# Performance work log

Hardware: AMD Instinct MI355X
Metric: run time of the kernel (lower is better)

## Reference

```python
import jax, jax.numpy as jnp
import numpy as np

B, S, D, HW = 256, 32, 512, 196


def setup_inputs() -> dict:
    key = jax.random.key(0)
    ks = jax.random.split(key, 34)
    n = lambda k, sh, s=1.0: jax.random.normal(k, sh, dtype=jnp.float32) * s
    w = 0.03  # xavier-ish scale for D=512 layers
    return {
        "words": n(ks[0], (B, S, D)),
        "question": n(ks[1], (B, 2 * D)),
        "know": n(ks[2], (B, D, HW)),
        "control0": n(ks[3], (B, D)),
        "memory0": n(ks[4], (B, D)),
        # ControlUnit
        "Wsc": n(ks[5], (2 * D, D), w), "bsc": jnp.zeros((D,), jnp.float32),
        "Wp": n(ks[6], (D, D), w), "bp": jnp.zeros((D,), jnp.float32),
        "Wcq": n(ks[7], (2 * D, D), w), "bcq": jnp.zeros((D,), jnp.float32),
        "wac": n(ks[8], (D, 1), w), "bac": jnp.zeros((1,), jnp.float32),
        # ReadUnit
        "Wm": n(ks[9], (D, D), w), "bm": jnp.zeros((D,), jnp.float32),
        "Wk": n(ks[10], (D, D), w), "bk": jnp.zeros((D,), jnp.float32),
        "Wc1": n(ks[11], (3 * D, D), w), "bc1": jnp.zeros((D,), jnp.float32),
        "Wc2": n(ks[12], (D, D), w), "bc2": jnp.zeros((D,), jnp.float32),
        "war": n(ks[13], (D, 1), w), "bar": jnp.zeros((1,), jnp.float32),
        # WriteUnit (self-attention variant)
        "Wwc": n(ks[14], (D, D), w), "bwc": jnp.zeros((D,), jnp.float32),
        "waw": n(ks[15], (D, 1), w), "baw": jnp.zeros((1,), jnp.float32),
        "Wwcat": n(ks[16], (3 * D, D), w), "bwcat": jnp.zeros((D,), jnp.float32),
    }


def reference(words, question, know, control0, memory0,
              Wsc, bsc, Wp, bp, Wcq, bcq, wac, bac,
              Wm, bm, Wk, bk, Wc1, bc1, Wc2, bc2, war, bar,
              Wwc, bwc, waw, baw, Wwcat, bwcat):
    # ---- ControlUnit (step 0) ----
    q = jnp.tanh(question @ Wsc + bsc)                    # [B,D]
    pa = q @ Wp + bp                                      # position_aware[0]
    cq = jnp.concatenate([control0, pa], axis=1) @ Wcq + bcq  # [B,D]
    logit_c = (cq[:, None, :] * words) @ wac + bac        # [B,S,1]
    attn_c = jax.nn.softmax(logit_c, axis=1)
    control = jnp.sum(attn_c * words, axis=1)             # [B,D]

    # ---- ReadUnit ----
    pm = memory0 @ Wm + bm                                # [B,D]
    pk = jnp.einsum('bdn,de->ben', know, Wk) + bk[None, :, None]  # [B,D,HW]
    pm_b = jnp.broadcast_to(pm[:, :, None], pk.shape)
    feat = jnp.concatenate([pm_b * pk, pk, pm_b], axis=1)  # [B,3D,HW]
    h = jax.nn.relu(jnp.einsum('bfn,fd->bnd', feat, Wc1) + bc1)  # [B,HW,D]
    h = h @ Wc2 + bc2                                     # [B,HW,D]
    logit_r = (h * control[:, None, :]) @ war + bar       # [B,HW,1]
    a_r = jax.nn.softmax(logit_r[..., 0], axis=1)          # [B,HW]
    read = jnp.einsum('bdn,bn->bd', know, a_r)            # [B,D]

    # ---- WriteUnit (self-attention over previous controls; T=1 at step 0) ----
    sc = control @ Wwc + bwc                              # [B,D]
    ctrl_prev = control0[:, :, None]                      # [B,D,T]
    logit_w = jnp.einsum('bdt,d->bt', sc[:, :, None] * ctrl_prev, waw[:, 0]) + baw  # [B,T]
    a_w = jax.nn.softmax(logit_w, axis=1)
    attn_mem = jnp.einsum('bdt,bt->bd', memory0[:, :, None], a_w)  # [B,D]
    concat = jnp.concatenate([read, memory0, attn_mem], axis=1)    # [B,3D]
    next_mem = concat @ Wwcat + bwcat                     # [B,D]

    return control, next_mem
```

## Files before the change

kernel.cpp:

```cpp
#include <hip/hip_runtime.h>
#include <hip/hip_bf16.h>
#include <math.h>

typedef __hip_bfloat16 bf16;
typedef __attribute__((ext_vector_type(8))) short s8v;
typedef __attribute__((ext_vector_type(4))) float f4v;

#define BB 256
#define SS 32
#define DD 512
#define HWN 196
#define AP 40

__device__ __forceinline__ float b2f(bf16 x){ return __bfloat162float(x); }
__device__ __forceinline__ bf16 f2b(float x){ return __float2bfloat16(x); }
__device__ __forceinline__ float us2f(unsigned short u){
    union { unsigned int i; float f; } t; t.i = ((unsigned int)u) << 16; return t.f;
}
template<int DT>
__device__ __forceinline__ float ldin(const void* p, size_t i){
    return DT ? b2f(((const bf16*)p)[i]) : ((const float*)p)[i];
}

__global__ void detect_k(const void* q, int* flag){
    __shared__ int cnt;
    if (threadIdx.x == 0) cnt = 0;
    __syncthreads();
    const unsigned short* u = (const unsigned short*)q;
    unsigned short v = u[threadIdx.x * 4];
    int e = (v >> 7) & 0xFF;
    atomicAdd(&cnt, (e >= 100 && e <= 140) ? 1 : 0);
    __syncthreads();
    if (threadIdx.x == 0) *flag = (cnt > 128) ? 1 : 0;
}

struct PJob { const void* s; const void* s2; bf16* d; int R, C, ldd, kofs, mode, nblk, boff; };
struct PrepP { PJob j[11]; const void* war; const void* bk; float* warf; float* bkf; };

template<int DT>
__global__ __launch_bounds__(256) void prep_k(PrepP P, const int* __restrict__ flag){
    if (*flag != DT) return;
    __shared__ float T[32][33];
    int bx = blockIdx.x;
    int ji = 0;
    #pragma unroll
    for (int i = 0; i < 11; ++i) if (bx >= P.j[i].boff) ji = i;
    PJob jb = P.j[ji];
    int t = bx - jb.boff;
    int tx = threadIdx.x & 31, ty = threadIdx.x >> 5;
    if (jb.mode == 3){
        for (int i = threadIdx.x; i < DD; i += 256){
            P.warf[i] = ldin<DT>(P.war, i);
            P.bkf[i]  = ldin<DT>(P.bk, i);
        }
        return;
    }
    int nrt = jb.R >> 5;
    int r0 = (t % nrt) << 5, c0 = (t / nrt) << 5;
    if (jb.mode == 2){
        for (int rr = ty; rr < 32; rr += 8)
            jb.d[(size_t)(r0 + rr) * jb.ldd + jb.kofs + c0 + tx] =
                f2b(ldin<DT>(jb.s, (size_t)(r0 + rr) * jb.C + c0 + tx));
        return;
    }
    for (int rr = ty; rr < 32; rr += 8){
        float v = ldin<DT>(jb.s, (size_t)(r0 + rr) * jb.C + c0 + tx);
        if (jb.mode == 1) v += ldin<DT>(jb.s2, (size_t)(r0 + rr) * jb.C + c0 + tx);
        T[rr][tx] = v;
    }
    __syncthreads();
    for (int rr = ty; rr < 32; rr += 8)
        jb.d[(size_t)(c0 + rr) * jb.ldd + jb.kofs + r0 + tx] = f2b(T[tx][rr]);
}

template<int DT>
__global__ void tr_know(const void* __restrict__ know, bf16* __restrict__ knowT, int b0,
                        const int* __restrict__ flag){
    if (*flag != DT) return;
    int bl = blockIdx.z, b = b0 + bl;
    int n0 = blockIdx.x * 32, g0 = blockIdx.y * 32;
    __shared__ float T[32][33];
    int tx = threadIdx.x & 31, ty = threadIdx.x >> 5;
    size_t base = (size_t)b * DD * HWN;
    for (int rr = ty; rr < 32; rr += 8){
        int n = n0 + tx;
        T[rr][tx] = (n < HWN) ? ldin<DT>(know, base + (size_t)(g0 + rr) * HWN + n) : 0.f;
    }
    __syncthreads();
    for (int rr = ty; rr < 32; rr += 8){
        int n = n0 + rr;
        if (n < HWN) knowT[((size_t)bl * HWN + n) * DD + g0 + tx] = f2b(T[tx][rr]);
    }
}

__global__ __launch_bounds__(256) void g1_mfma(const bf16* __restrict__ A,
                                               const bf16* __restrict__ BT,
                                               const float* __restrict__ bkf,
                                               bf16* __restrict__ C, int M){
    __shared__ __align__(16) bf16 As[128 * AP];
    __shared__ __align__(16) bf16 Bs[64 * AP];
    const int tid = threadIdx.x, lane = tid & 63, wave = tid >> 6;
    const int q = lane >> 4, mr = lane & 15;
    const int r0 = blockIdx.y * 128, c0 = blockIdx.x * 64;
    f4v acc[2][4];
    #pragma unroll
    for (int t = 0; t < 2; ++t)
        #pragma unroll
        for (int j = 0; j < 4; ++j){ f4v z = {0.f,0.f,0.f,0.f}; acc[t][j] = z; }
    for (int k0 = 0; k0 < DD; k0 += 32){
        #pragma unroll
        for (int cc = 0; cc < 2; ++cc){
            int c = tid + cc * 256;
            int row = c >> 2, ko = (c & 3) * 8;
            *(float4*)&As[row * AP + ko] =
                *(const float4*)(A + (size_t)(r0 + row) * DD + k0 + ko);
        }
        {
            int col = tid >> 2, ko = (tid & 3) * 8;
            *(float4*)&Bs[col * AP + ko] =
                *(const float4*)(BT + (size_t)(c0 + col) * DD + k0 + ko);
        }
        __syncthreads();
        s8v a0 = *(const s8v*)&As[(wave * 32 + mr) * AP + q * 8];
        s8v a1 = *(const s8v*)&As[(wave * 32 + 16 + mr) * AP + q * 8];
        #pragma unroll
        for (int j = 0; j < 4; ++j){
            s8v b = *(const s8v*)&Bs[(j * 16 + mr) * AP + q * 8];
            acc[0][j] = __builtin_amdgcn_mfma_f32_16x16x32_bf16(a0, b, acc[0][j], 0, 0, 0);
            acc[1][j] = __builtin_amdgcn_mfma_f32_16x16x32_bf16(a1, b, acc[1][j], 0, 0, 0);
        }
        __syncthreads();
    }
    #pragma unroll
    for (int t = 0; t < 2; ++t)
        #pragma unroll
        for (int j = 0; j < 4; ++j)
            #pragma unroll
            for (int i = 0; i < 4; ++i){
                int row = r0 + wave * 32 + t * 16 + q * 4 + i;
                int col = c0 + j * 16 + mr;
                C[(size_t)row * DD + col] = f2b(acc[t][j][i] + bkf[col]);
            }
}

__global__ __launch_bounds__(256) void g2_mfma(const bf16* __restrict__ Apk,
                                               const bf16* __restrict__ BT,
                                               const float* __restrict__ pmf,
                                               const float* __restrict__ t3b,
                                               const float* __restrict__ uf,
                                               float* __restrict__ logit,
                                               int b0, int M){
    __shared__ __align__(16) bf16 As[128 * AP];
    __shared__ __align__(16) bf16 Bs[64 * AP];
    const int tid = threadIdx.x, lane = tid & 63, wave = tid >> 6;
    const int q = lane >> 4, mr = lane & 15;
    const int r0 = blockIdx.y * 128, c0 = blockIdx.x * 64;
    f4v acc[2][4];
    #pragma unroll
    for (int t = 0; t < 2; ++t)
        #pragma unroll
        for (int j = 0; j < 4; ++j){ f4v z = {0.f,0.f,0.f,0.f}; acc[t][j] = z; }
    for (int k0 = 0; k0 < 2 * DD; k0 += 32){
        #pragma unroll
        for (int cc = 0; cc < 2; ++cc){
            int c = tid + cc * 256;
            int row = c >> 2, ko = (c & 3) * 8;
            int ksrc = (k0 + ko) & (DD - 1);
            float4 v = *(const float4*)(Apk + (size_t)(r0 + row) * DD + ksrc);
            alignas(16) bf16 h[8];
            *(float4*)h = v;
            if (k0 < DD){
                int b = b0 + (r0 + row) / HWN;
                const float* pp = pmf + (size_t)b * DD + ksrc;
                #pragma unroll
                for (int i2 = 0; i2 < 8; ++i2) h[i2] = f2b(b2f(h[i2]) * pp[i2]);
            }
            *(float4*)&As[row * AP + ko] = *(const float4*)h;
        }
        {
            int col = tid >> 2, ko = (tid & 3) * 8;
            *(float4*)&Bs[col * AP + ko] =
                *(const float4*)(BT + (size_t)(c0 + col) * (2 * DD) + k0 + ko);
        }
        __syncthreads();
        s8v a0 = *(const s8v*)&As[(wave * 32 + mr) * AP + q * 8];
        s8v a1 = *(const s8v*)&As[(wave * 32 + 16 + mr) * AP + q * 8];
        #pragma unroll
        for (int j = 0; j < 4; ++j){
            s8v b = *(const s8v*)&Bs[(j * 16 + mr) * AP + q * 8];
            acc[0][j] = __builtin_amdgcn_mfma_f32_16x16x32_bf16(a0, b, acc[0][j], 0, 0, 0);
            acc[1][j] = __builtin_amdgcn_mfma_f32_16x16x32_bf16(a1, b, acc[1][j], 0, 0, 0);
        }
        __syncthreads();
    }
    float part[2][4] = {};
    #pragma unroll
    for (int t = 0; t < 2; ++t)
        #pragma unroll
        for (int j = 0; j < 4; ++j)
            #pragma unroll
            for (int i = 0; i < 4; ++i){
                int row = r0 + wave * 32 + t * 16 + q * 4 + i;
                int b = b0 + row / HWN;
                int col = c0 + j * 16 + mr;
                float hv = acc[t][j][i] + t3b[(size_t)b * DD + col];
                part[t][i] += fmaxf(hv, 0.f) * uf[(size_t)b * DD + col];
            }
    #pragma unroll
    for (int t = 0; t < 2; ++t)
        #pragma unroll
        for (int i = 0; i < 4; ++i){
            float v = part[t][i];
            v += __shfl_xor(v, 1, 16);
            v += __shfl_xor(v, 2, 16);
            v += __shfl_xor(v, 4, 16);
            v += __shfl_xor(v, 8, 16);
            if (mr == 0){
                int row = r0 + wave * 32 + t * 16 + q * 4 + i;
                atomicAdd(&logit[(size_t)b0 * HWN + row], v);
            }
        }
}

struct SSeg { const void* A; int a_ws, lda, K, koff; };
struct SP {
    SSeg s[2]; int nseg;
    const bf16* BT; int ldb;
    const float* amul;
    const void* bias;
    float* C; int M, N, act;
};

template<int DT>
__global__ __launch_bounds__(256) void sgemm_k(SP p, const int* __restrict__ flag){
    if (*flag != DT) return;
    const int tid = threadIdx.x, lane = tid & 63, w = tid >> 6;
    const int q = lane >> 4, mr = lane & 15;
    const int n0 = blockIdx.x * 16, m0 = blockIdx.y * 64 + w * 16;
    f4v acc = {0.f,0.f,0.f,0.f};
    for (int sg = 0; sg < p.nseg; ++sg){
        const SSeg s = p.s[sg];
        const float* amul = (sg == 0) ? p.amul : nullptr;
        #pragma unroll 4
        for (int k0 = 0; k0 < s.K; k0 += 32){
            const int kk = k0 + q * 8;
            union { bf16 h[8]; s8v v; } a;
            if (s.a_ws || DT == 0){
                const float* Af = (const float*)s.A + (size_t)(m0 + mr) * s.lda + kk;
                float4 f0 = *(const float4*)Af;
                float4 f1 = *(const float4*)(Af + 4);
                float f[8] = {f0.x, f0.y, f0.z, f0.w, f1.x, f1.y, f1.z, f1.w};
                if (amul){
                    #pragma unroll
                    for (int j = 0; j < 8; ++j) f[j] *= amul[kk + j];
                }
                #pragma unroll
                for (int j = 0; j < 8; ++j) a.h[j] = f2b(f[j]);
            } else {
                a.v = *(const s8v*)((const bf16*)s.A + (size_t)(m0 + mr) * s.lda + kk);
                if (amul){
                    #pragma unroll
                    for (int j = 0; j < 8; ++j) a.h[j] = f2b(b2f(a.h[j]) * amul[kk + j]);
                }
            }
            s8v b = *(const s8v*)(p.BT + (size_t)(n0 + mr) * p.ldb + s.koff + kk);
            acc = __builtin_amdgcn_mfma_f32_16x16x32_bf16(a.v, b, acc, 0, 0, 0);
        }
    }
    #pragma unroll
    for (int i = 0; i < 4; ++i){
        int row = m0 + q * 4 + i, col = n0 + mr;
        float v = acc[i] + (p.bias ? ldin<DT>(p.bias, col) : 0.f);
        if (p.act == 1) v = tanhf(v);
        p.C[(size_t)row * p.N + col] = v;
    }
}

template<int DT>
__global__ __launch_bounds__(256) void attn_control_k(const float* __restrict__ cq,
                                                      const void* __restrict__ wac,
                                                      const void* __restrict__ bac,
                                                      const void* __restrict__ words,
                                                      float* __restrict__ control,
                                                      const int* __restrict__ flag){
    if (*flag != DT) return;
    const int b = blockIdx.x, tid = threadIdx.x;
    __shared__ float cw[DD];
    __shared__ float lg[SS];
    __shared__ float es[SS];
    for (int d = tid; d < DD; d += 256) cw[d] = cq[(size_t)b*DD + d] * ldin<DT>(wac, d);
    __syncthreads();
    int s = tid >> 3, l8 = tid & 7;
    float p = 0.f;
    for (int d = l8; d < DD; d += 8) p += cw[d] * ldin<DT>(words, ((size_t)b*SS + s)*DD + d);
    for (int off = 4; off; off >>= 1) p += __shfl_down(p, off, 8);
    if (l8 == 0) lg[s] = p + ldin<DT>(bac, 0);
    __syncthreads();
    if (tid == 0){
        float mx = -INFINITY;
        for (int i = 0; i < SS; ++i) mx = fmaxf(mx, lg[i]);
        float sm = 0.f;
        for (int i = 0; i < SS; ++i){ es[i] = expf(lg[i] - mx); sm += es[i]; }
        float inv = 1.f / sm;
        for (int i = 0; i < SS; ++i) es[i] *= inv;
    }
    __syncthreads();
    for (int d = tid; d < DD; d += 256){
        float c = 0.f;
        #pragma unroll 8
        for (int s2 = 0; s2 < SS; ++s2) c += es[s2] * ldin<DT>(words, ((size_t)b*SS + s2)*DD + d);
        control[(size_t)b*DD + d] = c;
    }
}

template<int DT>
__global__ __launch_bounds__(256) void vbias_k(const float* __restrict__ control,
                                               const void* __restrict__ war,
                                               const void* __restrict__ bc2,
                                               const void* __restrict__ bar,
                                               float* __restrict__ bias_r,
                                               const int* __restrict__ flag){
    if (*flag != DT) return;
    const int b = blockIdx.x, tid = threadIdx.x;
    __shared__ float red[256];
    float p = 0.f;
    for (int d = tid; d < DD; d += 256)
        p += ldin<DT>(bc2, d) * control[(size_t)b*DD + d] * ldin<DT>(war, d);
    red[tid] = p; __syncthreads();
    for (int off = 128; off; off >>= 1){ if (tid < off) red[tid] += red[tid + off]; __syncthreads(); }
    if (tid == 0) bias_r[b] = red[0] + ldin<DT>(bar, 0);
}

__global__ void init_logit_k(const float* __restrict__ bias_r, float* __restrict__ logit){
    int i = blockIdx.x * 256 + threadIdx.x;
    if (i < BB*HWN) logit[i] = bias_r[i / HWN];
}

template<int DT>
__global__ __launch_bounds__(256) void softmax_read_k(const float* __restrict__ logit,
                                                      const void* __restrict__ know,
                                                      float* __restrict__ readout,
                                                      const int* __restrict__ flag){
    if (*flag != DT) return;
    const int b = blockIdx.x, tid = threadIdx.x;
    __shared__ float a[HWN];
    __shared__ float red[256];
    float x = (tid < HWN) ? logit[(size_t)b*HWN + tid] : -INFINITY;
    red[tid] = x; __syncthreads();
    for (int off = 128; off; off >>= 1){ if (tid < off) red[tid] = fmaxf(red[tid], red[tid + off]); __syncthreads(); }
    float mx = red[0]; __syncthreads();
    float e = (tid < HWN) ? expf(x - mx) : 0.f;
    red[tid] = e; __syncthreads();
    for (int off = 128; off; off >>= 1){ if (tid < off) red[tid] += red[tid + off]; __syncthreads(); }
    float inv = 1.f / red[0];
    if (tid < HWN) a[tid] = e * inv;
    __syncthreads();
    for (int d = tid; d < DD; d += 256){
        size_t base = ((size_t)b*DD + d) * HWN;
        float sum = 0.f;
        if (DT){
            const ushort4* k4 = (const ushort4*)((const unsigned short*)know + base);
            #pragma unroll 7
            for (int c = 0; c < HWN/4; ++c){
                ushort4 u4 = k4[c];
                sum += a[4*c+0]*us2f(u4.x) + a[4*c+1]*us2f(u4.y)
                     + a[4*c+2]*us2f(u4.z) + a[4*c+3]*us2f(u4.w);
            }
        } else {
            const float4* k4 = (const float4*)((const float*)know + base);
            #pragma unroll 7
            for (int c = 0; c < HWN/4; ++c){
                float4 f4 = k4[c];
                sum += a[4*c+0]*f4.x + a[4*c+1]*f4.y + a[4*c+2]*f4.z + a[4*c+3]*f4.w;
            }
        }
        readout[(size_t)b*DD + d] = sum;
    }
}

template<int DT>
__global__ void writeout_k(const float* __restrict__ control, const float* __restrict__ nm,
                           void* __restrict__ out, const int* __restrict__ flag){
    if (*flag != DT) return;
    int i = blockIdx.x * 256 + threadIdx.x;
    const int NBD = BB * DD;
    float v;
    if (i < NBD) v = control[i];
    else if (i < 2*NBD) v = nm[i - NBD];
    else return;
    if (DT) ((bf16*)out)[i] = f2b(v);
    else    ((float*)out)[i] = v;
}

extern "C" void kernel_launch(void* const* d_in, const int* in_sizes, int n_in,
                              void* d_out, int out_size, void* d_ws, size_t ws_size,
                              hipStream_t stream){
    const void* words    = d_in[0];
    const void* question = d_in[1];
    const void* know     = d_in[2];
    const void* control0 = d_in[3];
    const void* memory0  = d_in[4];
    const void* Wsc = d_in[5];   const void* bsc = d_in[6];
    const void* Wp  = d_in[7];   const void* bp  = d_in[8];
    const void* Wcq = d_in[9];   const void* bcq = d_in[10];
    const void* wac = d_in[11];  const void* bac = d_in[12];
    const void* Wm  = d_in[13];  const void* bm  = d_in[14];
    const void* Wk  = d_in[15];  const void* bk  = d_in[16];
    const void* Wc1 = d_in[17];  const void* bc1 = d_in[18];
    const void* Wc2 = d_in[19];  const void* bc2 = d_in[20];
    const void* war = d_in[21];  const void* bar = d_in[22];
    const void* Wwcat = d_in[27]; const void* bwcat = d_in[28];

    int* flag = (int*)d_ws;
    float* F = ((float*)d_ws) + 16;
    const int NBD = BB * DD;
    float* q_   = F;
    float* pa   = F + 1*NBD;
    float* cq   = F + 2*NBD;
    float* ctrl = F + 3*NBD;
    float* pm   = F + 4*NBD;
    float* t3b  = F + 5*NBD;
    float* u_   = F + 6*NBD;
    float* rd   = F + 7*NBD;
    float* nm   = F + 8*NBD;
    float* bias_r = F + 9*NBD;
    float* logit  = bias_r + BB;
    float* warf   = logit + BB*HWN;
    float* bkf    = warf + DD;
    size_t off_f = 16 + 9*(size_t)NBD + BB + (size_t)BB*HWN + 2*DD;
    size_t byte_off = (off_f * 4 + 255) & ~(size_t)255;
    bf16* WB = (bf16*)((char*)d_ws + byte_off);
    bf16* WscT   = WB;
    bf16* WcqT   = WscT  + (size_t)DD*2*DD;
    bf16* Wc1T2  = WcqT  + (size_t)DD*2*DD;
    bf16* WwcatF = Wc1T2 + (size_t)DD*2*DD;
    bf16* WpT    = WwcatF+ (size_t)DD*2*DD;
    bf16* WmT    = WpT   + (size_t)DD*DD;
    bf16* Wc1t3T = WmT   + (size_t)DD*DD;
    bf16* WkT    = Wc1t3T+ (size_t)DD*DD;
    bf16* Wc2cv  = WkT   + (size_t)DD*DD;
    size_t big_off = (byte_off + ((size_t)DD*2*DD*4 + (size_t)DD*DD*5) * sizeof(bf16) + 255) & ~(size_t)255;

    size_t per_batch = (size_t)HWN * DD * sizeof(bf16) * 2;
    size_t avail = (ws_size > big_off) ? (ws_size - big_off) : 0;
    int CB = (int)(avail / per_batch);
    CB &= ~31;
    if (CB > BB) CB = BB;
    if (CB < 32) CB = 32;
    bf16* knowT = (bf16*)((char*)d_ws + big_off);
    bf16* pkT   = knowT + (size_t)CB * HWN * DD;

    dim3 blk(256);

    detect_k<<<dim3(1), blk, 0, stream>>>(question, flag);

    {
        PrepP P0; int bo = 0;
        auto J = [&](const void* s, const void* s2, bf16* d, int R, int C, int ldd,
                     int kofs, int mode, int idx){
            int nb = (mode == 3) ? 1 : ((R >> 5) * (C >> 5));
            P0.j[idx] = PJob{ s, s2, d, R, C, ldd, kofs, mode, nb, bo };
            bo += nb;
        };
        J(Wsc,   nullptr, WscT,   2*DD, DD, 2*DD, 0,   0, 0);
        J(Wp,    nullptr, WpT,    DD,   DD, DD,   0,   0, 1);
        J(Wcq,   nullptr, WcqT,   2*DD, DD, 2*DD, 0,   0, 2);
        J(Wm,    nullptr, WmT,    DD,   DD, DD,   0,   0, 3);
        J(Wc1,   nullptr, Wc1T2,  2*DD, DD, 2*DD, 0,   0, 4);
        J(nullptr,nullptr,Wc1t3T, DD,   DD, DD,   0,   0, 5);
        J(Wk,    nullptr, WkT,    DD,   DD, DD,   0,   0, 6);
        J(Wwcat, nullptr, WwcatF, DD,   DD, 2*DD, 0,   0, 7);
        J(nullptr,nullptr,WwcatF, DD,   DD, 2*DD, 512, 1, 8);
        J(Wc2,   nullptr, Wc2cv,  DD,   DD, DD,   0,   2, 9);
        J(nullptr,nullptr,nullptr,0,    0,  0,    0,   3, 10);
        P0.war = war; P0.bk = bk; P0.warf = warf; P0.bkf = bkf;
        PrepP P1 = P0;
        P0.j[5].s = (const void*)((const float*)Wc1 + (size_t)2*DD*DD);
        P1.j[5].s = (const void*)((const bf16*) Wc1 + (size_t)2*DD*DD);
        P0.j[8].s = (const void*)((const float*)Wwcat + (size_t)DD*DD);
        P1.j[8].s = (const void*)((const bf16*) Wwcat + (size_t)DD*DD);
        P0.j[8].s2 = (const void*)((const float*)Wwcat + (size_t)2*DD*DD);
        P1.j[8].s2 = (const void*)((const bf16*) Wwcat + (size_t)2*DD*DD);
        dim3 gp(bo);
        prep_k<0><<<gp, blk, 0, stream>>>(P0, flag);
        prep_k<1><<<gp, blk, 0, stream>>>(P1, flag);
    }

    dim3 g_s(DD/16, BB/64);
    SP p;
    #define LAUNCH_S(P) do { \
        sgemm_k<0><<<g_s, blk, 0, stream>>>(P, flag); \
        sgemm_k<1><<<g_s, blk, 0, stream>>>(P, flag); } while(0)

    p = SP{}; p.nseg = 1;
    p.s[0] = SSeg{ question, 0, 2*DD, 2*DD, 0 };
    p.BT = WscT; p.ldb = 2*DD; p.amul = nullptr;
    p.bias = bsc; p.C = q_; p.M = BB; p.N = DD; p.act = 1;
    LAUNCH_S(p);
    p = SP{}; p.nseg = 1;
    p.s[0] = SSeg{ q_, 1, DD, DD, 0 };
    p.BT = WpT; p.ldb = DD; p.amul = nullptr;
    p.bias = bp; p.C = pa; p.M = BB; p.N = DD; p.act = 0;
    LAUNCH_S(p);
    p = SP{}; p.nseg = 2;
    p.s[0] = SSeg{ control0, 0, DD, DD, 0 };
    p.s[1] = SSeg{ pa,       1, DD, DD, 512 };
    p.BT = WcqT; p.ldb = 2*DD; p.amul = nullptr;
    p.bias = bcq; p.C = cq; p.M = BB; p.N = DD; p.act = 0;
    LAUNCH_S(p);
    attn_control_k<0><<<dim3(BB), blk, 0, stream>>>(cq, wac, bac, words, ctrl, flag);
    attn_control_k<1><<<dim3(BB), blk, 0, stream>>>(cq, wac, bac, words, ctrl, flag);
    p = SP{}; p.nseg = 1;
    p.s[0] = SSeg{ memory0, 0, DD, DD, 0 };
    p.BT = WmT; p.ldb = DD; p.amul = nullptr;
    p.bias = bm; p.C = pm; p.M = BB; p.N = DD; p.act = 0;
    LAUNCH_S(p);
    p = SP{}; p.nseg = 1;
    p.s[0] = SSeg{ pm, 1, DD, DD, 0 };
    p.BT = Wc1t3T; p.ldb = DD; p.amul = nullptr;
    p.bias = bc1; p.C = t3b; p.M = BB; p.N = DD; p.act = 0;
    LAUNCH_S(p);
    vbias_k<0><<<dim3(BB), blk, 0, stream>>>(ctrl, war, bc2, bar, bias_r, flag);
    vbias_k<1><<<dim3(BB), blk, 0, stream>>>(ctrl, war, bc2, bar, bias_r, flag);
    p = SP{}; p.nseg = 1;
    p.s[0] = SSeg{ ctrl, 1, DD, DD, 0 };
    p.BT = Wc2cv; p.ldb = DD; p.amul = warf;
    p.bias = nullptr; p.C = u_; p.M = BB; p.N = DD; p.act = 0;
    LAUNCH_S(p);
    init_logit_k<<<dim3((BB*HWN + 255)/256), blk, 0, stream>>>(bias_r, logit);

    for (int b0 = 0; b0 < BB; b0 += CB){
        int cb = (b0 + CB <= BB) ? CB : (BB - b0);
        int M = cb * HWN;
        dim3 g_tr((HWN + 31)/32, DD/32, cb);
        tr_know<0><<<g_tr, blk, 0, stream>>>(know, knowT, b0, flag);
        tr_know<1><<<g_tr, blk, 0, stream>>>(know, knowT, b0, flag);
        dim3 g1g(DD/64, M/128);
        g1_mfma<<<g1g, blk, 0, stream>>>(knowT, WkT, bkf, pkT, M);
        g2_mfma<<<g1g, blk, 0, stream>>>(pkT, Wc1T2, pm, t3b, u_, logit, b0, M);
    }

    softmax_read_k<0><<<dim3(BB), blk, 0, stream>>>(logit, know, rd, flag);
    softmax_read_k<1><<<dim3(BB), blk, 0, stream>>>(logit, know, rd, flag);
    p = SP{}; p.nseg = 2;
    p.s[0] = SSeg{ rd,      1, DD, DD, 0 };
    p.s[1] = SSeg{ memory0, 0, DD, DD, 512 };
    p.BT = WwcatF; p.ldb = 2*DD; p.amul = nullptr;
    p.bias = bwcat; p.C = nm; p.M = BB; p.N = DD; p.act = 0;
    LAUNCH_S(p);
    writeout_k<0><<<dim3(2*NBD/256), blk, 0, stream>>>(ctrl, nm, d_out, flag);
    writeout_k<1><<<dim3(2*NBD/256), blk, 0, stream>>>(ctrl, nm, d_out, flag);
    #undef LAUNCH_S
}
```

Before: 677.6 us.

## Widen MFMA GEMM tiles to 128x128, swizzle block order, replace atomics with partials

```diff
diff --git a/kernel.cpp b/kernel.cpp
--- a/kernel.cpp
+++ b/kernel.cpp
@@ -96,17 +96,19 @@
 __global__ __launch_bounds__(256) void g1_mfma(const bf16* __restrict__ A,
                                                const bf16* __restrict__ BT,
                                                const float* __restrict__ bkf,
-                                               bf16* __restrict__ C, int M){
+                                               bf16* __restrict__ C, int nR, int swz){
     __shared__ __align__(16) bf16 As[128 * AP];
-    __shared__ __align__(16) bf16 Bs[64 * AP];
+    __shared__ __align__(16) bf16 Bs[128 * AP];
     const int tid = threadIdx.x, lane = tid & 63, wave = tid >> 6;
     const int q = lane >> 4, mr = lane & 15;
-    const int r0 = blockIdx.y * 128, c0 = blockIdx.x * 64;
-    f4v acc[2][4];
+    int idb = blockIdx.x, rt, ct;
+    if (swz){ rt = idb % nR; ct = idb / nR; } else { ct = idb & 3; rt = idb >> 2; }
+    const int r0 = rt * 128, c0 = ct * 128;
+    f4v acc[2][8];
     #pragma unroll
     for (int t = 0; t < 2; ++t)
         #pragma unroll
-        for (int j = 0; j < 4; ++j){ f4v z = {0.f,0.f,0.f,0.f}; acc[t][j] = z; }
+        for (int j = 0; j < 8; ++j){ f4v z = {0.f,0.f,0.f,0.f}; acc[t][j] = z; }
     for (int k0 = 0; k0 < DD; k0 += 32){
         #pragma unroll
         for (int cc = 0; cc < 2; ++cc){
@@ -115,8 +117,10 @@
             *(float4*)&As[row * AP + ko] =
                 *(const float4*)(A + (size_t)(r0 + row) * DD + k0 + ko);
         }
-        {
-            int col = tid >> 2, ko = (tid & 3) * 8;
+        #pragma unroll
+        for (int cc = 0; cc < 2; ++cc){
+            int c = tid + cc * 256;
+            int col = c >> 2, ko = (c & 3) * 8;
             *(float4*)&Bs[col * AP + ko] =
                 *(const float4*)(BT + (size_t)(c0 + col) * DD + k0 + ko);
         }
@@ -124,7 +128,7 @@
         s8v a0 = *(const s8v*)&As[(wave * 32 + mr) * AP + q * 8];
         s8v a1 = *(const s8v*)&As[(wave * 32 + 16 + mr) * AP + q * 8];
         #pragma unroll
-        for (int j = 0; j < 4; ++j){
+        for (int j = 0; j < 8; ++j){
             s8v b = *(const s8v*)&Bs[(j * 16 + mr) * AP + q * 8];
             acc[0][j] = __builtin_amdgcn_mfma_f32_16x16x32_bf16(a0, b, acc[0][j], 0, 0, 0);
             acc[1][j] = __builtin_amdgcn_mfma_f32_16x16x32_bf16(a1, b, acc[1][j], 0, 0, 0);
@@ -134,7 +138,7 @@
     #pragma unroll
     for (int t = 0; t < 2; ++t)
         #pragma unroll
-        for (int j = 0; j < 4; ++j)
+        for (int j = 0; j < 8; ++j)
             #pragma unroll
             for (int i = 0; i < 4; ++i){
                 int row = r0 + wave * 32 + t * 16 + q * 4 + i;
@@ -148,18 +152,20 @@
                                                const float* __restrict__ pmf,
                                                const float* __restrict__ t3b,
                                                const float* __restrict__ uf,
-                                               float* __restrict__ logit,
-                                               int b0, int M){
+                                               float* __restrict__ lpart,
+                                               int b0, int nR, int swz){
     __shared__ __align__(16) bf16 As[128 * AP];
-    __shared__ __align__(16) bf16 Bs[64 * AP];
+    __shared__ __align__(16) bf16 Bs[128 * AP];
     const int tid = threadIdx.x, lane = tid & 63, wave = tid >> 6;
     const int q = lane >> 4, mr = lane & 15;
-    const int r0 = blockIdx.y * 128, c0 = blockIdx.x * 64;
-    f4v acc[2][4];
+    int idb = blockIdx.x, rt, ct;
+    if (swz){ rt = idb % nR; ct = idb / nR; } else { ct = idb & 3; rt = idb >> 2; }
+    const int r0 = rt * 128, c0 = ct * 128;
+    f4v acc[2][8];
     #pragma unroll
     for (int t = 0; t < 2; ++t)
         #pragma unroll
-        for (int j = 0; j < 4; ++j){ f4v z = {0.f,0.f,0.f,0.f}; acc[t][j] = z; }
+        for (int j = 0; j < 8; ++j){ f4v z = {0.f,0.f,0.f,0.f}; acc[t][j] = z; }
     for (int k0 = 0; k0 < 2 * DD; k0 += 32){
         #pragma unroll
         for (int cc = 0; cc < 2; ++cc){
@@ -177,8 +183,10 @@
             }
             *(float4*)&As[row * AP + ko] = *(const float4*)h;
         }
-        {
-            int col = tid >> 2, ko = (tid & 3) * 8;
+        #pragma unroll
+        for (int cc = 0; cc < 2; ++cc){
+            int c = tid + cc * 256;
+            int col = c >> 2, ko = (c & 3) * 8;
             *(float4*)&Bs[col * AP + ko] =
                 *(const float4*)(BT + (size_t)(c0 + col) * (2 * DD) + k0 + ko);
         }
@@ -186,7 +194,7 @@
         s8v a0 = *(const s8v*)&As[(wave * 32 + mr) * AP + q * 8];
         s8v a1 = *(const s8v*)&As[(wave * 32 + 16 + mr) * AP + q * 8];
         #pragma unroll
-        for (int j = 0; j < 4; ++j){
+        for (int j = 0; j < 8; ++j){
             s8v b = *(const s8v*)&Bs[(j * 16 + mr) * AP + q * 8];
             acc[0][j] = __builtin_amdgcn_mfma_f32_16x16x32_bf16(a0, b, acc[0][j], 0, 0, 0);
             acc[1][j] = __builtin_amdgcn_mfma_f32_16x16x32_bf16(a1, b, acc[1][j], 0, 0, 0);
@@ -197,7 +205,7 @@
     #pragma unroll
     for (int t = 0; t < 2; ++t)
         #pragma unroll
-        for (int j = 0; j < 4; ++j)
+        for (int j = 0; j < 8; ++j)
             #pragma unroll
             for (int i = 0; i < 4; ++i){
                 int row = r0 + wave * 32 + t * 16 + q * 4 + i;
@@ -217,9 +225,17 @@
             v += __shfl_xor(v, 8, 16);
             if (mr == 0){
                 int row = r0 + wave * 32 + t * 16 + q * 4 + i;
-                atomicAdd(&logit[(size_t)b0 * HWN + row], v);
-            }
-        }
+                lpart[(size_t)ct * (BB * HWN) + (size_t)b0 * HWN + row] = v;
+            }
+        }
+}
+
+__global__ void reduce_logit_k(const float* __restrict__ lpart, const float* __restrict__ bias_r,
+                               float* __restrict__ logit){
+    int i = blockIdx.x * 256 + threadIdx.x;
+    const int T = BB * HWN;
+    if (i < T)
+        logit[i] = bias_r[i / HWN] + lpart[i] + lpart[T + i] + lpart[2*T + i] + lpart[3*T + i];
 }
 
 struct SSeg { const void* A; int a_ws, lda, K, koff; };
@@ -331,11 +347,6 @@
     if (tid == 0) bias_r[b] = red[0] + ldin<DT>(bar, 0);
 }
 
-__global__ void init_logit_k(const float* __restrict__ bias_r, float* __restrict__ logit){
-    int i = blockIdx.x * 256 + threadIdx.x;
-    if (i < BB*HWN) logit[i] = bias_r[i / HWN];
-}
-
 template<int DT>
 __global__ __launch_bounds__(256) void softmax_read_k(const float* __restrict__ logit,
                                                       const void* __restrict__ know,
@@ -427,7 +438,8 @@
     float* logit  = bias_r + BB;
     float* warf   = logit + BB*HWN;
     float* bkf    = warf + DD;
-    size_t off_f = 16 + 9*(size_t)NBD + BB + (size_t)BB*HWN + 2*DD;
+    float* lpart  = bkf + DD;
+    size_t off_f = 16 + 9*(size_t)NBD + BB + (size_t)BB*HWN + 2*DD + 4*(size_t)BB*HWN;
     size_t byte_off = (off_f * 4 + 255) & ~(size_t)255;
     bf16* WB = (bf16*)((char*)d_ws + byte_off);
     bf16* WscT   = WB;
@@ -527,7 +539,6 @@
     p.BT = Wc2cv; p.ldb = DD; p.amul = warf;
     p.bias = nullptr; p.C = u_; p.M = BB; p.N = DD; p.act = 0;
     LAUNCH_S(p);
-    init_logit_k<<<dim3((BB*HWN + 255)/256), blk, 0, stream>>>(bias_r, logit);
 
     for (int b0 = 0; b0 < BB; b0 += CB){
         int cb = (b0 + CB <= BB) ? CB : (BB - b0);
@@ -535,11 +546,14 @@
         dim3 g_tr((HWN + 31)/32, DD/32, cb);
         tr_know<0><<<g_tr, blk, 0, stream>>>(know, knowT, b0, flag);
         tr_know<1><<<g_tr, blk, 0, stream>>>(know, knowT, b0, flag);
-        dim3 g1g(DD/64, M/128);
-        g1_mfma<<<g1g, blk, 0, stream>>>(knowT, WkT, bkf, pkT, M);
-        g2_mfma<<<g1g, blk, 0, stream>>>(pkT, Wc1T2, pm, t3b, u_, logit, b0, M);
-    }
-
+        int nR = M / 128;
+        int swz = (nR % 8 == 0) ? 1 : 0;
+        dim3 gflat(4 * nR);
+        g1_mfma<<<gflat, blk, 0, stream>>>(knowT, WkT, bkf, pkT, nR, swz);
+        g2_mfma<<<gflat, blk, 0, stream>>>(pkT, Wc1T2, pm, t3b, u_, lpart, b0, nR, swz);
+    }
+
+    reduce_logit_k<<<dim3((BB*HWN + 255)/256), blk, 0, stream>>>(lpart, bias_r, logit);
     softmax_read_k<0><<<dim3(BB), blk, 0, stream>>>(logit, know, rd, flag);
     softmax_read_k<1><<<dim3(BB), blk, 0, stream>>>(logit, know, rd, flag);
     p = SP{}; p.nseg = 2;
```

After: 718.7 us. 1.06x slower.

## Merge dtype-templated kernel pairs, swizzle GEMM tiles, replace logit atomics with partials

Applied to the files above, without the earlier changes.

```diff
diff --git a/kernel.cpp b/kernel.cpp
--- a/kernel.cpp
+++ b/kernel.cpp
@@ -17,9 +17,8 @@
 __device__ __forceinline__ float us2f(unsigned short u){
     union { unsigned int i; float f; } t; t.i = ((unsigned int)u) << 16; return t.f;
 }
-template<int DT>
-__device__ __forceinline__ float ldin(const void* p, size_t i){
-    return DT ? b2f(((const bf16*)p)[i]) : ((const float*)p)[i];
+__device__ __forceinline__ float ldin(int dt, const void* p, size_t i){
+    return dt ? b2f(((const bf16*)p)[i]) : ((const float*)p)[i];
 }
 
 __global__ void detect_k(const void* q, int* flag){
@@ -34,24 +33,26 @@
     if (threadIdx.x == 0) *flag = (cnt > 128) ? 1 : 0;
 }
 
-struct PJob { const void* s; const void* s2; bf16* d; int R, C, ldd, kofs, mode, nblk, boff; };
+struct PJob { const void* s; const void* s_b; const void* s2; const void* s2_b;
+              bf16* d; int R, C, ldd, kofs, mode, boff; };
 struct PrepP { PJob j[11]; const void* war; const void* bk; float* warf; float* bkf; };
 
-template<int DT>
 __global__ __launch_bounds__(256) void prep_k(PrepP P, const int* __restrict__ flag){
-    if (*flag != DT) return;
+    const int dt = *flag;
     __shared__ float T[32][33];
     int bx = blockIdx.x;
     int ji = 0;
     #pragma unroll
     for (int i = 0; i < 11; ++i) if (bx >= P.j[i].boff) ji = i;
     PJob jb = P.j[ji];
+    const void* src  = dt ? jb.s_b  : jb.s;
+    const void* src2 = dt ? jb.s2_b : jb.s2;
     int t = bx - jb.boff;
     int tx = threadIdx.x & 31, ty = threadIdx.x >> 5;
     if (jb.mode == 3){
         for (int i = threadIdx.x; i < DD; i += 256){
-            P.warf[i] = ldin<DT>(P.war, i);
-            P.bkf[i]  = ldin<DT>(P.bk, i);
+            P.warf[i] = ldin(dt, P.war, i);
+            P.bkf[i]  = ldin(dt, P.bk, i);
         }
         return;
     }
@@ -60,12 +61,12 @@
     if (jb.mode == 2){
         for (int rr = ty; rr < 32; rr += 8)
             jb.d[(size_t)(r0 + rr) * jb.ldd + jb.kofs + c0 + tx] =
-                f2b(ldin<DT>(jb.s, (size_t)(r0 + rr) * jb.C + c0 + tx));
+                f2b(ldin(dt, src, (size_t)(r0 + rr) * jb.C + c0 + tx));
         return;
     }
     for (int rr = ty; rr < 32; rr += 8){
-        float v = ldin<DT>(jb.s, (size_t)(r0 + rr) * jb.C + c0 + tx);
-        if (jb.mode == 1) v += ldin<DT>(jb.s2, (size_t)(r0 + rr) * jb.C + c0 + tx);
+        float v = ldin(dt, src, (size_t)(r0 + rr) * jb.C + c0 + tx);
+        if (jb.mode == 1) v += ldin(dt, src2, (size_t)(r0 + rr) * jb.C + c0 + tx);
         T[rr][tx] = v;
     }
     __syncthreads();
@@ -73,10 +74,9 @@
         jb.d[(size_t)(c0 + rr) * jb.ldd + jb.kofs + r0 + tx] = f2b(T[tx][rr]);
 }
 
-template<int DT>
 __global__ void tr_know(const void* __restrict__ know, bf16* __restrict__ knowT, int b0,
                         const int* __restrict__ flag){
-    if (*flag != DT) return;
+    const int dt = *flag;
     int bl = blockIdx.z, b = b0 + bl;
     int n0 = blockIdx.x * 32, g0 = blockIdx.y * 32;
     __shared__ float T[32][33];
@@ -84,7 +84,7 @@
     size_t base = (size_t)b * DD * HWN;
     for (int rr = ty; rr < 32; rr += 8){
         int n = n0 + tx;
-        T[rr][tx] = (n < HWN) ? ldin<DT>(know, base + (size_t)(g0 + rr) * HWN + n) : 0.f;
+        T[rr][tx] = (n < HWN) ? ldin(dt, know, base + (size_t)(g0 + rr) * HWN + n) : 0.f;
     }
     __syncthreads();
     for (int rr = ty; rr < 32; rr += 8){
@@ -93,15 +93,21 @@
     }
 }
 
+__device__ __forceinline__ void tile_decode(int idb, int swz, int& rt, int& ct){
+    if (swz){ int g = idb >> 6, w = idb & 63; rt = g * 8 + (w & 7); ct = w >> 3; }
+    else    { ct = idb & 7; rt = idb >> 3; }
+}
+
 __global__ __launch_bounds__(256) void g1_mfma(const bf16* __restrict__ A,
                                                const bf16* __restrict__ BT,
                                                const float* __restrict__ bkf,
-                                               bf16* __restrict__ C, int M){
+                                               bf16* __restrict__ C, int swz){
     __shared__ __align__(16) bf16 As[128 * AP];
     __shared__ __align__(16) bf16 Bs[64 * AP];
     const int tid = threadIdx.x, lane = tid & 63, wave = tid >> 6;
     const int q = lane >> 4, mr = lane & 15;
-    const int r0 = blockIdx.y * 128, c0 = blockIdx.x * 64;
+    int rt, ct; tile_decode(blockIdx.x, swz, rt, ct);
+    const int r0 = rt * 128, c0 = ct * 64;
     f4v acc[2][4];
     #pragma unroll
     for (int t = 0; t < 2; ++t)
@@ -148,13 +154,14 @@
                                                const float* __restrict__ pmf,
                                                const float* __restrict__ t3b,
                                                const float* __restrict__ uf,
-                                               float* __restrict__ logit,
-                                               int b0, int M){
+                                               float* __restrict__ lpart,
+                                               int b0, int swz){
     __shared__ __align__(16) bf16 As[128 * AP];
     __shared__ __align__(16) bf16 Bs[64 * AP];
     const int tid = threadIdx.x, lane = tid & 63, wave = tid >> 6;
     const int q = lane >> 4, mr = lane & 15;
-    const int r0 = blockIdx.y * 128, c0 = blockIdx.x * 64;
+    int rt, ct; tile_decode(blockIdx.x, swz, rt, ct);
+    const int r0 = rt * 128, c0 = ct * 64;
     f4v acc[2][4];
     #pragma unroll
     for (int t = 0; t < 2; ++t)
@@ -217,9 +224,21 @@
             v += __shfl_xor(v, 8, 16);
             if (mr == 0){
                 int row = r0 + wave * 32 + t * 16 + q * 4 + i;
-                atomicAdd(&logit[(size_t)b0 * HWN + row], v);
-            }
-        }
+                lpart[(size_t)ct * (BB * HWN) + (size_t)b0 * HWN + row] = v;
+            }
+        }
+}
+
+__global__ void reduce_logit_k(const float* __restrict__ lpart, const float* __restrict__ bias_r,
+                               float* __restrict__ logit){
+    int i = blockIdx.x * 256 + threadIdx.x;
+    const int T = BB * HWN;
+    if (i < T){
+        float s = bias_r[i / HWN];
+        #pragma unroll
+        for (int c = 0; c < 8; ++c) s += lpart[(size_t)c * T + i];
+        logit[i] = s;
+    }
 }
 
 struct SSeg { const void* A; int a_ws, lda, K, koff; };
@@ -231,9 +250,8 @@
     float* C; int M, N, act;
 };
 
-template<int DT>
 __global__ __launch_bounds__(256) void sgemm_k(SP p, const int* __restrict__ flag){
-    if (*flag != DT) return;
+    const int dt = *flag;
     const int tid = threadIdx.x, lane = tid & 63, w = tid >> 6;
     const int q = lane >> 4, mr = lane & 15;
     const int n0 = blockIdx.x * 16, m0 = blockIdx.y * 64 + w * 16;
@@ -245,7 +263,7 @@
         for (int k0 = 0; k0 < s.K; k0 += 32){
             const int kk = k0 + q * 8;
             union { bf16 h[8]; s8v v; } a;
-            if (s.a_ws || DT == 0){
+            if (s.a_ws || dt == 0){
                 const float* Af = (const float*)s.A + (size_t)(m0 + mr) * s.lda + kk;
                 float4 f0 = *(const float4*)Af;
                 float4 f1 = *(const float4*)(Af + 4);
@@ -270,31 +288,30 @@
     #pragma unroll
     for (int i = 0; i < 4; ++i){
         int row = m0 + q * 4 + i, col = n0 + mr;
-        float v = acc[i] + (p.bias ? ldin<DT>(p.bias, col) : 0.f);
+        float v = acc[i] + (p.bias ? ldin(dt, p.bias, col) : 0.f);
         if (p.act == 1) v = tanhf(v);
         p.C[(size_t)row * p.N + col] = v;
     }
 }
 
-template<int DT>
 __global__ __launch_bounds__(256) void attn_control_k(const float* __restrict__ cq,
                                                       const void* __restrict__ wac,
                                                       const void* __restrict__ bac,
                                                       const void* __restrict__ words,
                                                       float* __restrict__ control,
                                                       const int* __restrict__ flag){
-    if (*flag != DT) return;
+    const int dt = *flag;
     const int b = blockIdx.x, tid = threadIdx.x;
     __shared__ float cw[DD];
     __shared__ float lg[SS];
     __shared__ float es[SS];
-    for (int d = tid; d < DD; d += 256) cw[d] = cq[(size_t)b*DD + d] * ldin<DT>(wac, d);
+    for (int d = tid; d < DD; d += 256) cw[d] = cq[(size_t)b*DD + d] * ldin(dt, wac, d);
     __syncthreads();
     int s = tid >> 3, l8 = tid & 7;
     float p = 0.f;
-    for (int d = l8; d < DD; d += 8) p += cw[d] * ldin<DT>(words, ((size_t)b*SS + s)*DD + d);
+    for (int d = l8; d < DD; d += 8) p += cw[d] * ldin(dt, words, ((size_t)b*SS + s)*DD + d);
     for (int off = 4; off; off >>= 1) p += __shfl_down(p, off, 8);
-    if (l8 == 0) lg[s] = p + ldin<DT>(bac, 0);
+    if (l8 == 0) lg[s] = p + ldin(dt, bac, 0);
     __syncthreads();
     if (tid == 0){
         float mx = -INFINITY;
@@ -308,40 +325,33 @@
     for (int d = tid; d < DD; d += 256){
         float c = 0.f;
         #pragma unroll 8
-        for (int s2 = 0; s2 < SS; ++s2) c += es[s2] * ldin<DT>(words, ((size_t)b*SS + s2)*DD + d);
+        for (int s2 = 0; s2 < SS; ++s2) c += es[s2] * ldin(dt, words, ((size_t)b*SS + s2)*DD + d);
         control[(size_t)b*DD + d] = c;
     }
 }
 
-template<int DT>
 __global__ __launch_bounds__(256) void vbias_k(const float* __restrict__ control,
                                                const void* __restrict__ war,
                                                const void* __restrict__ bc2,
                                                const void* __restrict__ bar,
                                                float* __restrict__ bias_r,
                                                const int* __restrict__ flag){
-    if (*flag != DT) return;
+    const int dt = *flag;
     const int b = blockIdx.x, tid = threadIdx.x;
     __shared__ float red[256];
     float p = 0.f;
     for (int d = tid; d < DD; d += 256)
-        p += ldin<DT>(bc2, d) * control[(size_t)b*DD + d] * ldin<DT>(war, d);
+        p += ldin(dt, bc2, d) * control[(size_t)b*DD + d] * ldin(dt, war, d);
     red[tid] = p; __syncthreads();
     for (int off = 128; off; off >>= 1){ if (tid < off) red[tid] += red[tid + off]; __syncthreads(); }
-    if (tid == 0) bias_r[b] = red[0] + ldin<DT>(bar, 0);
-}
-
-__global__ void init_logit_k(const float* __restrict__ bias_r, float* __restrict__ logit){
-    int i = blockIdx.x * 256 + threadIdx.x;
-    if (i < BB*HWN) logit[i] = bias_r[i / HWN];
-}
-
-template<int DT>
+    if (tid == 0) bias_r[b] = red[0] + ldin(dt, bar, 0);
+}
+
 __global__ __launch_bounds__(256) void softmax_read_k(const float* __restrict__ logit,
                                                       const void* __restrict__ know,
                                                       float* __restrict__ readout,
                                                       const int* __restrict__ flag){
-    if (*flag != DT) return;
+    const int dt = *flag;
     const int b = blockIdx.x, tid = threadIdx.x;
     __shared__ float a[HWN];
     __shared__ float red[256];
@@ -358,7 +368,7 @@
     for (int d = tid; d < DD; d += 256){
         size_t base = ((size_t)b*DD + d) * HWN;
         float sum = 0.f;
-        if (DT){
+        if (dt){
             const ushort4* k4 = (const ushort4*)((const unsigned short*)know + base);
             #pragma unroll 7
             for (int c = 0; c < HWN/4; ++c){
@@ -378,17 +388,16 @@
     }
 }
 
-template<int DT>
 __global__ void writeout_k(const float* __restrict__ control, const float* __restrict__ nm,
                            void* __restrict__ out, const int* __restrict__ flag){
-    if (*flag != DT) return;
+    const int dt = *flag;
     int i = blockIdx.x * 256 + threadIdx.x;
     const int NBD = BB * DD;
     float v;
     if (i < NBD) v = control[i];
     else if (i < 2*NBD) v = nm[i - NBD];
     else return;
-    if (DT) ((bf16*)out)[i] = f2b(v);
+    if (dt) ((bf16*)out)[i] = f2b(v);
     else    ((float*)out)[i] = v;
 }
 
@@ -427,7 +436,8 @@
     float* logit  = bias_r + BB;
     float* warf   = logit + BB*HWN;
     float* bkf    = warf + DD;
-    size_t off_f = 16 + 9*(size_t)NBD + BB + (size_t)BB*HWN + 2*DD;
+    float* lpart  = bkf + DD;
+    size_t off_f = 16 + 9*(size_t)NBD + BB + (size_t)BB*HWN + 2*DD + 8*(size_t)BB*HWN;
     size_t byte_off = (off_f * 4 + 255) & ~(size_t)255;
     bf16* WB = (bf16*)((char*)d_ws + byte_off);
     bf16* WscT   = WB;
@@ -455,100 +465,90 @@
     detect_k<<<dim3(1), blk, 0, stream>>>(question, flag);
 
     {
-        PrepP P0; int bo = 0;
-        auto J = [&](const void* s, const void* s2, bf16* d, int R, int C, int ldd,
-                     int kofs, int mode, int idx){
+        PrepP P; int bo = 0;
+        auto J = [&](const void* s, const void* sb, const void* s2, const void* s2b,
+                     bf16* d, int R, int C, int ldd, int kofs, int mode, int idx){
             int nb = (mode == 3) ? 1 : ((R >> 5) * (C >> 5));
-            P0.j[idx] = PJob{ s, s2, d, R, C, ldd, kofs, mode, nb, bo };
+            P.j[idx] = PJob{ s, sb, s2, s2b, d, R, C, ldd, kofs, mode, bo };
             bo += nb;
         };
-        J(Wsc,   nullptr, WscT,   2*DD, DD, 2*DD, 0,   0, 0);
-        J(Wp,    nullptr, WpT,    DD,   DD, DD,   0,   0, 1);
-        J(Wcq,   nullptr, WcqT,   2*DD, DD, 2*DD, 0,   0, 2);
-        J(Wm,    nullptr, WmT,    DD,   DD, DD,   0,   0, 3);
-        J(Wc1,   nullptr, Wc1T2,  2*DD, DD, 2*DD, 0,   0, 4);
-        J(nullptr,nullptr,Wc1t3T, DD,   DD, DD,   0,   0, 5);
-        J(Wk,    nullptr, WkT,    DD,   DD, DD,   0,   0, 6);
-        J(Wwcat, nullptr, WwcatF, DD,   DD, 2*DD, 0,   0, 7);
-        J(nullptr,nullptr,WwcatF, DD,   DD, 2*DD, 512, 1, 8);
-        J(Wc2,   nullptr, Wc2cv,  DD,   DD, DD,   0,   2, 9);
-        J(nullptr,nullptr,nullptr,0,    0,  0,    0,   3, 10);
-        P0.war = war; P0.bk = bk; P0.warf = warf; P0.bkf = bkf;
-        PrepP P1 = P0;
-        P0.j[5].s = (const void*)((const float*)Wc1 + (size_t)2*DD*DD);
-        P1.j[5].s = (const void*)((const bf16*) Wc1 + (size_t)2*DD*DD);
-        P0.j[8].s = (const void*)((const float*)Wwcat + (size_t)DD*DD);
-        P1.j[8].s = (const void*)((const bf16*) Wwcat + (size_t)DD*DD);
-        P0.j[8].s2 = (const void*)((const float*)Wwcat + (size_t)2*DD*DD);
-        P1.j[8].s2 = (const void*)((const bf16*) Wwcat + (size_t)2*DD*DD);
-        dim3 gp(bo);
-        prep_k<0><<<gp, blk, 0, stream>>>(P0, flag);
-        prep_k<1><<<gp, blk, 0, stream>>>(P1, flag);
+        const void* Wc1t3_f = (const void*)((const float*)Wc1 + (size_t)2*DD*DD);
+        const void* Wc1t3_b = (const void*)((const bf16*) Wc1 + (size_t)2*DD*DD);
+        const void* Ww1_f = (const void*)((const float*)Wwcat + (size_t)DD*DD);
+        const void* Ww1_b = (const void*)((const bf16*) Wwcat + (size_t)DD*DD);
+        const void* Ww2_f = (const void*)((const float*)Wwcat + (size_t)2*DD*DD);
+        const void* Ww2_b = (const void*)((const bf16*) Wwcat + (size_t)2*DD*DD);
+        J(Wsc,   Wsc,   nullptr, nullptr, WscT,   2*DD, DD, 2*DD, 0,   0, 0);
+        J(Wp,    Wp,    nullptr, nullptr, WpT,    DD,   DD, DD,   0,   0, 1);
+        J(Wcq,   Wcq,   nullptr, nullptr, WcqT,   2*DD, DD, 2*DD, 0,   0, 2);
+        J(Wm,    Wm,    nullptr, nullptr, WmT,    DD,   DD, DD,   0,   0, 3);
+        J(Wc1,   Wc1,   nullptr, nullptr, Wc1T2,  2*DD, DD, 2*DD, 0,   0, 4);
+        J(Wc1t3_f, Wc1t3_b, nullptr, nullptr, Wc1t3T, DD, DD, DD, 0,   0, 5);
+        J(Wk,    Wk,    nullptr, nullptr, WkT,    DD,   DD, DD,   0,   0, 6);
+        J(Wwcat, Wwcat, nullptr, nullptr, WwcatF, DD,   DD, 2*DD, 0,   0, 7);
+        J(Ww1_f, Ww1_b, Ww2_f,   Ww2_b,   WwcatF, DD,   DD, 2*DD, 512, 1, 8);
+        J(Wc2,   Wc2,   nullptr, nullptr, Wc2cv,  DD,   DD, DD,   0,   2, 9);
+        J(nullptr,nullptr,nullptr,nullptr,nullptr,0,    0,  0,    0,   3, 10);
+        P.war = war; P.bk = bk; P.warf = warf; P.bkf = bkf;
+        prep_k<<<dim3(bo), blk, 0, stream>>>(P, flag);
     }
 
     dim3 g_s(DD/16, BB/64);
     SP p;
-    #define LAUNCH_S(P) do { \
-        sgemm_k<0><<<g_s, blk, 0, stream>>>(P, flag); \
-        sgemm_k<1><<<g_s, blk, 0, stream>>>(P, flag); } while(0)
 
     p = SP{}; p.nseg = 1;
     p.s[0] = SSeg{ question, 0, 2*DD, 2*DD, 0 };
     p.BT = WscT; p.ldb = 2*DD; p.amul = nullptr;
     p.bias = bsc; p.C = q_; p.M = BB; p.N = DD; p.act = 1;
-    LAUNCH_S(p);
+    sgemm_k<<<g_s, blk, 0, stream>>>(p, flag);
     p = SP{}; p.nseg = 1;
     p.s[0] = SSeg{ q_, 1, DD, DD, 0 };
     p.BT = WpT; p.ldb = DD; p.amul = nullptr;
     p.bias = bp; p.C = pa; p.M = BB; p.N = DD; p.act = 0;
-    LAUNCH_S(p);
+    sgemm_k<<<g_s, blk, 0, stream>>>(p, flag);
     p = SP{}; p.nseg = 2;
     p.s[0] = SSeg{ control0, 0, DD, DD, 0 };
     p.s[1] = SSeg{ pa,       1, DD, DD, 512 };
     p.BT = WcqT; p.ldb = 2*DD; p.amul = nullptr;
     p.bias = bcq; p.C = cq; p.M = BB; p.N = DD; p.act = 0;
-    LAUNCH_S(p);
-    attn_control_k<0><<<dim3(BB), blk, 0, stream>>>(cq, wac, bac, words, ctrl, flag);
-    attn_control_k<1><<<dim3(BB), blk, 0, stream>>>(cq, wac, bac, words, ctrl, flag);
+    sgemm_k<<<g_s, blk, 0, stream>>>(p, flag);
+    attn_control_k<<<dim3(BB), blk, 0, stream>>>(cq, wac, bac, words, ctrl, flag);
     p = SP{}; p.nseg = 1;
     p.s[0] = SSeg{ memory0, 0, DD, DD, 0 };
     p.BT = WmT; p.ldb = DD; p.amul = nullptr;
     p.bias = bm; p.C = pm; p.M = BB; p.N = DD; p.act = 0;
-    LAUNCH_S(p);
+    sgemm_k<<<g_s, blk, 0, stream>>>(p, flag);
     p = SP{}; p.nseg = 1;
     p.s[0] = SSeg{ pm, 1, DD, DD, 0 };
     p.BT = Wc1t3T; p.ldb = DD; p.amul = nullptr;
     p.bias = bc1; p.C = t3b; p.M = BB; p.N = DD; p.act = 0;
-    LAUNCH_S(p);
-    vbias_k<0><<<dim3(BB), blk, 0, stream>>>(ctrl, war, bc2, bar, bias_r, flag);
-    vbias_k<1><<<dim3(BB), blk, 0, stream>>>(ctrl, war, bc2, bar, bias_r, flag);
+    sgemm_k<<<g_s, blk, 0, stream>>>(p, flag);
+    vbias_k<<<dim3(BB), blk, 0, stream>>>(ctrl, war, bc2, bar, bias_r, flag);
     p = SP{}; p.nseg = 1;
     p.s[0] = SSeg{ ctrl, 1, DD, DD, 0 };
     p.BT = Wc2cv; p.ldb = DD; p.amul = warf;
     p.bias = nullptr; p.C = u_; p.M = BB; p.N = DD; p.act = 0;
-    LAUNCH_S(p);
-    init_logit_k<<<dim3((BB*HWN + 255)/256), blk, 0, stream>>>(bias_r, logit);
+    sgemm_k<<<g_s, blk, 0, stream>>>(p, flag);
 
     for (int b0 = 0; b0 < BB; b0 += CB){
         int cb = (b0 + CB <= BB) ? CB : (BB - b0);
         int M = cb * HWN;
         dim3 g_tr((HWN + 31)/32, DD/32, cb);
-        tr_know<0><<<g_tr, blk, 0, stream>>>(know, knowT, b0, flag);
-        tr_know<1><<<g_tr, blk, 0, stream>>>(know, knowT, b0, flag);
-        dim3 g1g(DD/64, M/128);
-        g1_mfma<<<g1g, blk, 0, stream>>>(knowT, WkT, bkf, pkT, M);
-        g2_mfma<<<g1g, blk, 0, stream>>>(pkT, Wc1T2, pm, t3b, u_, logit, b0, M);
-    }
-
-    softmax_read_k<0><<<dim3(BB), blk, 0, stream>>>(logit, know, rd, flag);
-    softmax_read_k<1><<<dim3(BB), blk, 0, stream>>>(logit, know, rd, flag);
+        tr_know<<<g_tr, blk, 0, stream>>>(know, knowT, b0, flag);
+        int nR = M / 128;
+        int swz = (nR % 8 == 0) ? 1 : 0;
+        dim3 gflat(8 * nR);
+        g1_mfma<<<gflat, blk, 0, stream>>>(knowT, WkT, bkf, pkT, swz);
+        g2_mfma<<<gflat, blk, 0, stream>>>(pkT, Wc1T2, pm, t3b, u_, lpart, b0, swz);
+    }
+
+    reduce_logit_k<<<dim3((BB*HWN + 255)/256), blk, 0, stream>>>(lpart, bias_r, logit);
+    softmax_read_k<<<dim3(BB), blk, 0, stream>>>(logit, know, rd, flag);
     p = SP{}; p.nseg = 2;
     p.s[0] = SSeg{ rd,      1, DD, DD, 0 };
     p.s[1] = SSeg{ memory0, 0, DD, DD, 512 };
     p.BT = WwcatF; p.ldb = 2*DD; p.amul = nullptr;
     p.bias = bwcat; p.C = nm; p.M = BB; p.N = DD; p.act = 0;
-    LAUNCH_S(p);
-    writeout_k<0><<<dim3(2*NBD/256), blk, 0, stream>>>(ctrl, nm, d_out, flag);
-    writeout_k<1><<<dim3(2*NBD/256), blk, 0, stream>>>(ctrl, nm, d_out, flag);
-    #undef LAUNCH_S
-}
+    sgemm_k<<<g_s, blk, 0, stream>>>(p, flag);
+    writeout_k<<<dim3(2*NBD/256), blk, 0, stream>>>(ctrl, nm, d_out, flag);
+}
```

Measured after the change: 633.6 us. 1.07x faster.
